# Optimization experiments

Hardware: AMD Instinct MI355X
Metric: run time of the kernel (lower is better)

## Reference

```python
import jax, jax.numpy as jnp
import numpy as np

B, L, G, D = 4096, 64, 8, 128
N_ITEMS, N_USERS, N_RATINGS = 100000, 50000, 5


def setup_inputs() -> dict:
    key = jax.random.key(0)
    ks = jax.random.split(key, 16)
    s = jnp.float32(0.02)
    return dict(
        nodes=jax.random.randint(ks[0], (B, G), 0, N_USERS),
        history_u=jax.random.randint(ks[1], (B, L), 0, N_ITEMS),
        history_r=jax.random.randint(ks[2], (B, L), 0, N_RATINGS),
        hist_len=jax.random.randint(ks[3], (B,), 0, L),
        v2e_weight=jax.random.normal(ks[4], (N_ITEMS, D), dtype=jnp.float32) * s,
        u2e_weight=jax.random.normal(ks[5], (N_USERS, D), dtype=jnp.float32) * s,
        r2e_weight=jax.random.normal(ks[6], (N_RATINGS, D), dtype=jnp.float32) * s,
        W1=jax.random.normal(ks[7], (2 * D, D), dtype=jnp.float32) * s,
        b1=jnp.zeros((D,), jnp.float32),
        W2=jax.random.normal(ks[8], (D, D), dtype=jnp.float32) * s,
        b2=jnp.zeros((D,), jnp.float32),
        att1_W=jax.random.normal(ks[9], (2 * D, D), dtype=jnp.float32) * s,
        att1_b=jnp.zeros((D,), jnp.float32),
        att2_W=jax.random.normal(ks[10], (D, D), dtype=jnp.float32) * s,
        att2_b=jnp.zeros((D,), jnp.float32),
        att3_W=jax.random.normal(ks[11], (D, 1), dtype=jnp.float32) * s,
        att3_b=jnp.zeros((1,), jnp.float32),
        ge_W=jax.random.normal(ks[12], (D, D), dtype=jnp.float32) * s,
        ge_b=jnp.zeros((D,), jnp.float32),
    )


def reference(nodes, history_u, history_r, hist_len,
              v2e_weight, u2e_weight, r2e_weight,
              W1, b1, W2, b2,
              att1_W, att1_b, att2_W, att2_b, att3_W, att3_b,
              ge_W, ge_b):
    lengths = hist_len + 1                      # ensure >=1 valid history entry per group
    e_uv = v2e_weight[history_u]                # [B, L, D] item-history gather
    e_r = r2e_weight[history_r]                 # [B, L, D] rating gather
    members = u2e_weight[nodes]                 # [B, G, D] member gather
    # Group_Embedding: pool members to one rep per group
    g = jax.nn.relu(members.mean(axis=1) @ ge_W + ge_b)            # [B, D]
    # per-history 2-layer MLP (w_r1, w_r2)
    x = jax.nn.relu(jnp.concatenate([e_uv, e_r], axis=-1) @ W1 + b1)
    o = jax.nn.relu(x @ W2 + b2)                # [B, L, D] o_history
    # Attention: cat(o_history, group_rep) -> relu -> relu -> scalar, softmax over L
    g_rep = jnp.broadcast_to(g[:, None, :], o.shape)               # [B, L, D]
    a = jax.nn.relu(jnp.concatenate([o, g_rep], axis=-1) @ att1_W + att1_b)
    a = jax.nn.relu(a @ att2_W + att2_b)
    logits = (a @ att3_W + att3_b)[..., 0]      # [B, L]
    mask = jnp.arange(L)[None, :] < lengths[:, None]
    logits = jnp.where(mask, logits, jnp.float32(-1e9))
    att = jax.nn.softmax(logits, axis=-1) * mask                   # ragged masked softmax
    # torch.mm(o_history.t(), att_w).t() == attention-weighted reduce over L
    return jnp.einsum('bl,bld->bd', att, o)     # [B, D]
```

## Files before the change

### kernel.cpp

```cpp
#include <hip/hip_runtime.h>
#include <hip/hip_bf16.h>

#define DD 128
#define TILE_BYTES 32768
#define WS_R_OFF   196608
#define WS_GB_OFF  199168

typedef __attribute__((ext_vector_type(8))) short bf16x8;
typedef __attribute__((ext_vector_type(4))) float f32x4;

__device__ inline unsigned short f2bf(float f) {
  unsigned u = __float_as_uint(f);
  return (unsigned short)((u + 0x7fffu + ((u >> 16) & 1u)) >> 16);
}

__device__ inline void async16(void* ldsp, const void* gp) {
  __builtin_amdgcn_global_load_lds(
      (const __attribute__((address_space(1))) void*)gp,
      (__attribute__((address_space(3))) void*)ldsp, 16, 0, 0);
}

__device__ inline void fill_w(char* slot, const char* src, int tid) {
  int w = tid >> 6, lane = tid & 63;
  #pragma unroll
  for (int i = 0; i < 8; ++i) {
    int ofs = ((i << 2) + w) << 10;
    async16(slot + ofs, src + ofs + lane * 16);
  }
}

__device__ inline bf16x8 ldfrag(const char* buf, int rowbase, int kk, int lane) {
  int row = rowbase + (lane & 15);
  int off = (row << 8) + (kk << 6) + (lane & 48);
  off ^= (row & 7) << 4;
  return *(const bf16x8*)(buf + off);
}

__device__ inline bf16x8 ldAg(const float* rp, int kk, int lane) {
  const float4* p = (const float4*)(rp + (kk << 5) + ((lane >> 4) << 3));
  float4 f0 = p[0], f1 = p[1];
  bf16x8 r;
  r[0] = (short)f2bf(f0.x); r[1] = (short)f2bf(f0.y);
  r[2] = (short)f2bf(f0.z); r[3] = (short)f2bf(f0.w);
  r[4] = (short)f2bf(f1.x); r[5] = (short)f2bf(f1.y);
  r[6] = (short)f2bf(f1.z); r[7] = (short)f2bf(f1.w);
  return r;
}

__device__ inline uint2 pack4(float v0, float v1, float v2, float v3) {
  return make_uint2((unsigned)f2bf(v0) | ((unsigned)f2bf(v1) << 16),
                    (unsigned)f2bf(v2) | ((unsigned)f2bf(v3) << 16));
}

#define MFMA(a, b, c) __builtin_amdgcn_mfma_f32_16x16x32_bf16((a), (b), (c), 0, 0, 0)

__global__ __launch_bounds__(256) void prep_weights(
    const float* __restrict__ W1, const float* __restrict__ W2,
    const float* __restrict__ a1W, const float* __restrict__ a2W,
    const float* __restrict__ geW,
    const float* __restrict__ r2e, const float* __restrict__ b1,
    unsigned short* __restrict__ wsw, float* __restrict__ Rp) {
  int gid = blockIdx.x * 256 + threadIdx.x;
  if (gid < 12288) {
    int tile = gid >> 11, idx = gid & 2047;
    int row = idx >> 4, slot = idx & 15;
    int slot2 = slot ^ (row & 7);
    const float* W; int kb;
    switch (tile) {
      case 0:  W = W1;  kb = 0;   break;
      case 1:  W = W2;  kb = 0;   break;
      case 2:  W = a1W; kb = 0;   break;
      case 3:  W = a2W; kb = 0;   break;
      case 4:  W = geW; kb = 0;   break;
      default: W = a1W; kb = 128; break;
    }
    unsigned pk[4];
    #pragma unroll
    for (int p = 0; p < 4; ++p) {
      unsigned short lo = f2bf(W[(size_t)(kb + slot2 * 8 + 2 * p) * DD + row]);
      unsigned short hi = f2bf(W[(size_t)(kb + slot2 * 8 + 2 * p + 1) * DD + row]);
      pk[p] = (unsigned)lo | ((unsigned)hi << 16);
    }
    *(uint4*)(wsw + (size_t)tile * 16384 + (size_t)idx * 8) =
        make_uint4(pk[0], pk[1], pk[2], pk[3]);
  } else {
    int t = gid - 12288;
    for (int idx = t; idx < 640; idx += 256) {
      int r = idx >> 7, d = idx & 127;
      float s = b1[d];
      for (int k = 0; k < 128; ++k)
        s = fmaf(r2e[r * DD + k], W1[(size_t)(DD + k) * DD + d], s);
      Rp[idx] = s;
    }
  }
}

__global__ __launch_bounds__(256, 2) void prep_gb(
    const int* __restrict__ nodes, const float* __restrict__ u2e,
    const float* __restrict__ geb, const float* __restrict__ a1b,
    const char* __restrict__ tiles, float* __restrict__ gbv) {
  __shared__ char mean_s[4096];
  __shared__ char g_s[4096];
  __shared__ char wslot[32768];
  __shared__ int nodes_s[128];
  int tid = threadIdx.x, w = tid >> 6, lane = tid & 63;
  int b0 = blockIdx.x * 16;
  if (tid < 128) nodes_s[tid] = nodes[b0 * 8 + tid];
  fill_w(wslot, tiles + 4 * TILE_BYTES, tid);
  __syncthreads();
  for (int idx = tid; idx < 2048; idx += 256) {
    int row = idx >> 7, d = idx & 127;
    float m = 0.f;
    #pragma unroll
    for (int j = 0; j < 8; ++j)
      m += u2e[(size_t)nodes_s[row * 8 + j] * DD + d];
    m *= 0.125f;
    int off = ((row << 8) + (d << 1)) ^ ((row & 7) << 4);
    *(unsigned short*)(mean_s + off) = f2bf(m);
  }
  __syncthreads();
  int cb = lane & 15, rb = (lane >> 4) << 2;
  f32x4 acc[2] = {(f32x4)(0.f), (f32x4)(0.f)};
  #pragma unroll
  for (int kk = 0; kk < 4; ++kk) {
    bf16x8 a = ldfrag(mean_s, 0, kk, lane);
    #pragma unroll
    for (int nf = 0; nf < 2; ++nf) {
      bf16x8 b = ldfrag(wslot, w * 32 + nf * 16, kk, lane);
      acc[nf] = MFMA(a, b, acc[nf]);
    }
  }
  __syncthreads();
  fill_w(wslot, tiles + 5 * TILE_BYTES, tid);
  #pragma unroll
  for (int nf = 0; nf < 2; ++nf) {
    int col = w * 32 + nf * 16 + cb;
    float gb2 = geb[col];
    #pragma unroll
    for (int j = 0; j < 4; ++j) {
      int row = rb + j;
      float v = fmaxf(acc[nf][j] + gb2, 0.f);
      int off = ((row << 8) + (col << 1)) ^ ((row & 7) << 4);
      *(unsigned short*)(g_s + off) = f2bf(v);
    }
  }
  __syncthreads();
  acc[0] = (f32x4)(0.f); acc[1] = (f32x4)(0.f);
  #pragma unroll
  for (int kk = 0; kk < 4; ++kk) {
    bf16x8 a = ldfrag(g_s, 0, kk, lane);
    #pragma unroll
    for (int nf = 0; nf < 2; ++nf) {
      bf16x8 b = ldfrag(wslot, w * 32 + nf * 16, kk, lane);
      acc[nf] = MFMA(a, b, acc[nf]);
    }
  }
  #pragma unroll
  for (int nf = 0; nf < 2; ++nf) {
    int col = w * 32 + nf * 16 + cb;
    float bb = a1b[col];
    #pragma unroll
    for (int j = 0; j < 4; ++j)
      gbv[(size_t)(b0 + rb + j) * DD + col] = acc[nf][j] + bb;
  }
}

__device__ inline void gemmWX(f32x4 acc[8], const char* Wt, const char* Xt,
                              int mfw, int nlw, int lane) {
  #pragma unroll
  for (int kk = 0; kk < 4; ++kk) {
    bf16x8 bf0 = ldfrag(Xt, nlw * 32, kk, lane);
    bf16x8 bf1 = ldfrag(Xt, nlw * 32 + 16, kk, lane);
    #pragma unroll
    for (int mf = 0; mf < 4; ++mf) {
      bf16x8 a = ldfrag(Wt, mfw * 64 + mf * 16, kk, lane);
      acc[mf * 2]     = MFMA(a, bf0, acc[mf * 2]);
      acc[mf * 2 + 1] = MFMA(a, bf1, acc[mf * 2 + 1]);
    }
  }
}

__global__ __launch_bounds__(512, 1) void main_kernel(
    const int* __restrict__ hu, const int* __restrict__ hr,
    const int* __restrict__ hlen,
    const float* __restrict__ v2e,
    const float* __restrict__ b2, const float* __restrict__ a2b,
    const float* __restrict__ a3W, const float* __restrict__ a3b,
    const char* __restrict__ tiles, const float* __restrict__ Rp,
    const float* __restrict__ gbv, float* __restrict__ out) {
  __shared__ char smem[163840];
  char* W1s = smem;
  char* W2s = smem + 32768;
  char* A1s = smem + 65536;
  char* A2s = smem + 98304;
  char* XA  = smem + 131072;
  char* XB  = smem + 147456;

  const int tid = threadIdx.x, lane = tid & 63;
  const int wv = tid >> 6;
  const int rowsel = wv >> 2;
  const int w4 = wv & 3;
  const int mfw = w4 >> 1, nlw = w4 & 1;
  const int cb = lane & 15, g = lane >> 4;
  char* X = rowsel ? XB : XA;

  #pragma unroll
  for (int i = 0; i < 4; ++i) {
    int ofs = (i * 8 + wv) << 10;
    async16(W1s + ofs, tiles + ofs + lane * 16);
    async16(W2s + ofs, tiles + TILE_BYTES + ofs + lane * 16);
    async16(A1s + ofs, tiles + 2 * TILE_BYTES + ofs + lane * 16);
    async16(A2s + ofs, tiles + 3 * TILE_BYTES + ofs + lane * 16);
  }
  const float a3bv = a3b[0];

  const int l0 = nlw * 32 + cb, l1 = l0 + 16;
  const int rbase = blockIdx.x * 16;
  int r = rbase + rowsel;
  int hu0 = hu[r * 64 + l0], hu1 = hu[r * 64 + l1];
  int hr0 = hr[r * 64 + l0], hr1 = hr[r * 64 + l1];
  __syncthreads();

  for (int p = 0; p < 8; ++p) {
    int hu0n = 0, hu1n = 0, hr0n = 0, hr1n = 0;
    if (p < 7) {
      int rn = r + 2;
      hu0n = hu[rn * 64 + l0]; hu1n = hu[rn * 64 + l1];
      hr0n = hr[rn * 64 + l0]; hr1n = hr[rn * 64 + l1];
    }

    f32x4 acc[8];
    #pragma unroll
    for (int i = 0; i < 8; ++i) acc[i] = (f32x4)(0.f);

    {
      const float* rp0 = v2e + (size_t)hu0 * DD;
      const float* rp1 = v2e + (size_t)hu1 * DD;
      #pragma unroll
      for (int kk = 0; kk < 4; ++kk) {
        bf16x8 bf0 = ldAg(rp0, kk, lane);
        bf16x8 bf1 = ldAg(rp1, kk, lane);
        #pragma unroll
        for (int mf = 0; mf < 4; ++mf) {
          bf16x8 a = ldfrag(W1s, mfw * 64 + mf * 16, kk, lane);
          acc[mf * 2]     = MFMA(a, bf0, acc[mf * 2]);
          acc[mf * 2 + 1] = MFMA(a, bf1, acc[mf * 2 + 1]);
        }
      }
    }
    #pragma unroll
    for (int mf = 0; mf < 4; ++mf) {
      int f0 = mfw * 64 + mf * 16 + g * 4;
      float4 r0 = *(const float4*)(Rp + hr0 * DD + f0);
      float4 r1 = *(const float4*)(Rp + hr1 * DD + f0);
      f32x4 v0 = acc[mf * 2], v1 = acc[mf * 2 + 1];
      uint2 p0 = pack4(fmaxf(v0[0] + r0.x, 0.f), fmaxf(v0[1] + r0.y, 0.f),
                       fmaxf(v0[2] + r0.z, 0.f), fmaxf(v0[3] + r0.w, 0.f));
      uint2 p1 = pack4(fmaxf(v1[0] + r1.x, 0.f), fmaxf(v1[1] + r1.y, 0.f),
                       fmaxf(v1[2] + r1.z, 0.f), fmaxf(v1[3] + r1.w, 0.f));
      int o0 = ((l0 << 8) + (f0 << 1)) ^ ((l0 & 7) << 4);
      int o1 = ((l1 << 8) + (f0 << 1)) ^ ((l1 & 7) << 4);
      *(uint2*)(X + o0) = p0;
      *(uint2*)(X + o1) = p1;
    }
    __syncthreads();

    #pragma unroll
    for (int i = 0; i < 8; ++i) acc[i] = (f32x4)(0.f);
    gemmWX(acc, W2s, X, mfw, nlw, lane);
    __syncthreads();
    uint2 opk[8];
    #pragma unroll
    for (int mf = 0; mf < 4; ++mf) {
      int f0 = mfw * 64 + mf * 16 + g * 4;
      float4 bb = *(const float4*)(b2 + f0);
      f32x4 v0 = acc[mf * 2], v1 = acc[mf * 2 + 1];
      uint2 p0 = pack4(fmaxf(v0[0] + bb.x, 0.f), fmaxf(v0[1] + bb.y, 0.f),
                       fmaxf(v0[2] + bb.z, 0.f), fmaxf(v0[3] + bb.w, 0.f));
      uint2 p1 = pack4(fmaxf(v1[0] + bb.x, 0.f), fmaxf(v1[1] + bb.y, 0.f),
                       fmaxf(v1[2] + bb.z, 0.f), fmaxf(v1[3] + bb.w, 0.f));
      opk[mf * 2] = p0; opk[mf * 2 + 1] = p1;
      int o0 = ((l0 << 8) + (f0 << 1)) ^ ((l0 & 7) << 4);
      int o1 = ((l1 << 8) + (f0 << 1)) ^ ((l1 & 7) << 4);
      *(uint2*)(X + o0) = p0;
      *(uint2*)(X + o1) = p1;
    }
    __syncthreads();

    #pragma unroll
    for (int i = 0; i < 8; ++i) acc[i] = (f32x4)(0.f);
    gemmWX(acc, A1s, X, mfw, nlw, lane);
    __syncthreads();
    #pragma unroll
    for (int mf = 0; mf < 4; ++mf) {
      int f0 = mfw * 64 + mf * 16 + g * 4;
      float4 gv = *(const float4*)(gbv + (size_t)r * DD + f0);
      f32x4 v0 = acc[mf * 2], v1 = acc[mf * 2 + 1];
      uint2 p0 = pack4(fmaxf(v0[0] + gv.x, 0.f), fmaxf(v0[1] + gv.y, 0.f),
                       fmaxf(v0[2] + gv.z, 0.f), fmaxf(v0[3] + gv.w, 0.f));
      uint2 p1 = pack4(fmaxf(v1[0] + gv.x, 0.f), fmaxf(v1[1] + gv.y, 0.f),
                       fmaxf(v1[2] + gv.z, 0.f), fmaxf(v1[3] + gv.w, 0.f));
      int o0 = ((l0 << 8) + (f0 << 1)) ^ ((l0 & 7) << 4);
      int o1 = ((l1 << 8) + (f0 << 1)) ^ ((l1 & 7) << 4);
      *(uint2*)(X + o0) = p0;
      *(uint2*)(X + o1) = p1;
    }
    __syncthreads();

    #pragma unroll
    for (int i = 0; i < 8; ++i) acc[i] = (f32x4)(0.f);
    gemmWX(acc, A2s, X, mfw, nlw, lane);
    __syncthreads();

    {
      float s0 = 0.f, s1 = 0.f;
      #pragma unroll
      for (int mf = 0; mf < 4; ++mf) {
        int f0 = mfw * 64 + mf * 16 + g * 4;
        float4 ab = *(const float4*)(a2b + f0);
        float4 aw = *(const float4*)(a3W + f0);
        f32x4 v0 = acc[mf * 2], v1 = acc[mf * 2 + 1];
        s0 = fmaf(fmaxf(v0[0] + ab.x, 0.f), aw.x, s0);
        s0 = fmaf(fmaxf(v0[1] + ab.y, 0.f), aw.y, s0);
        s0 = fmaf(fmaxf(v0[2] + ab.z, 0.f), aw.z, s0);
        s0 = fmaf(fmaxf(v0[3] + ab.w, 0.f), aw.w, s0);
        s1 = fmaf(fmaxf(v1[0] + ab.x, 0.f), aw.x, s1);
        s1 = fmaf(fmaxf(v1[1] + ab.y, 0.f), aw.y, s1);
        s1 = fmaf(fmaxf(v1[2] + ab.z, 0.f), aw.z, s1);
        s1 = fmaf(fmaxf(v1[3] + ab.w, 0.f), aw.w, s1);
      }
      s0 += __shfl_xor(s0, 16); s0 += __shfl_xor(s0, 32);
      s1 += __shfl_xor(s1, 16); s1 += __shfl_xor(s1, 32);
      if (g == 0) {
        *(float*)(X + mfw * 256 + l0 * 4) = s0;
        *(float*)(X + mfw * 256 + l1 * 4) = s1;
      }
    }
    __syncthreads();

    if (w4 == 0) {
      int l = lane;
      float lv = *(const float*)(X + l * 4) + *(const float*)(X + 256 + l * 4) + a3bv;
      int len = hlen[r] + 1;
      bool valid = l < len;
      if (!valid) lv = -1e30f;
      float m = lv;
      #pragma unroll
      for (int off = 32; off; off >>= 1) m = fmaxf(m, __shfl_xor(m, off));
      float pe = valid ? expf(lv - m) : 0.f;
      float s = pe;
      #pragma unroll
      for (int off = 32; off; off >>= 1) s += __shfl_xor(s, off);
      *(float*)(X + 512 + l * 4) = pe / s;
    }
    __syncthreads();

    {
      float att0 = *(const float*)(X + 512 + l0 * 4);
      float att1 = *(const float*)(X + 512 + l1 * 4);
      float pr[4][4];
      #pragma unroll
      for (int mf = 0; mf < 4; ++mf) {
        uint2 q0 = opk[mf * 2], q1 = opk[mf * 2 + 1];
        pr[mf][0] = att0 * __uint_as_float(q0.x << 16)
                  + att1 * __uint_as_float(q1.x << 16);
        pr[mf][1] = att0 * __uint_as_float(q0.x & 0xffff0000u)
                  + att1 * __uint_as_float(q1.x & 0xffff0000u);
        pr[mf][2] = att0 * __uint_as_float(q0.y << 16)
                  + att1 * __uint_as_float(q1.y << 16);
        pr[mf][3] = att0 * __uint_as_float(q0.y & 0xffff0000u)
                  + att1 * __uint_as_float(q1.y & 0xffff0000u);
      }
      #pragma unroll
      for (int m = 1; m < 16; m <<= 1) {
        #pragma unroll
        for (int mf = 0; mf < 4; ++mf) {
          pr[mf][0] += __shfl_xor(pr[mf][0], m);
          pr[mf][1] += __shfl_xor(pr[mf][1], m);
          pr[mf][2] += __shfl_xor(pr[mf][2], m);
          pr[mf][3] += __shfl_xor(pr[mf][3], m);
        }
      }
      if (cb == 0) {
        #pragma unroll
        for (int mf = 0; mf < 4; ++mf) {
          int f0 = mfw * 64 + mf * 16 + g * 4;
          float* rd = (float*)(X + 1024 + nlw * 512);
          rd[f0 + 0] = pr[mf][0];
          rd[f0 + 1] = pr[mf][1];
          rd[f0 + 2] = pr[mf][2];
          rd[f0 + 3] = pr[mf][3];
        }
      }
    }
    __syncthreads();

    if (tid < 128 || (tid >= 256 && tid < 384)) {
      int d = tid & 127;
      out[(size_t)r * DD + d] = *(const float*)(X + 1024 + d * 4)
                              + *(const float*)(X + 1536 + d * 4);
    }
    __syncthreads();

    hu0 = hu0n; hu1 = hu1n; hr0 = hr0n; hr1 = hr1n;
    r += 2;
  }
}

extern "C" void kernel_launch(void* const* d_in, const int* in_sizes, int n_in,
                              void* d_out, int out_size, void* d_ws, size_t ws_size,
                              hipStream_t stream) {
  const int*   nodes = (const int*)d_in[0];
  const int*   hu    = (const int*)d_in[1];
  const int*   hr    = (const int*)d_in[2];
  const int*   hlen  = (const int*)d_in[3];
  const float* v2e   = (const float*)d_in[4];
  const float* u2e   = (const float*)d_in[5];
  const float* r2e   = (const float*)d_in[6];
  const float* W1    = (const float*)d_in[7];
  const float* b1    = (const float*)d_in[8];
  const float* W2    = (const float*)d_in[9];
  const float* b2    = (const float*)d_in[10];
  const float* a1W   = (const float*)d_in[11];
  const float* a1b   = (const float*)d_in[12];
  const float* a2W   = (const float*)d_in[13];
  const float* a2b   = (const float*)d_in[14];
  const float* a3W   = (const float*)d_in[15];
  const float* a3b   = (const float*)d_in[16];
  const float* geW   = (const float*)d_in[17];
  const float* geb   = (const float*)d_in[18];
  float* out = (float*)d_out;

  unsigned short* wsw = (unsigned short*)d_ws;
  const char* tiles = (const char*)d_ws;
  float* Rp  = (float*)((char*)d_ws + WS_R_OFF);
  float* gbv = (float*)((char*)d_ws + WS_GB_OFF);

  prep_weights<<<49, 256, 0, stream>>>(W1, W2, a1W, a2W, geW, r2e, b1, wsw, Rp);
  prep_gb<<<256, 256, 0, stream>>>(nodes, u2e, geb, a1b, tiles, gbv);
  main_kernel<<<256, 512, 0, stream>>>(
      hu, hr, hlen, v2e, b2, a2b, a3W, a3b, tiles, Rp, gbv, out);
}
```

Measured before the change: 121.3 us.

## Double block to 16 waves, split features per wave, compute softmax per wave

The main kernel now launches 1024 threads per block, so each row is handled by 8 waves that each own 32 output features instead of 64. This halves per-wave MFMA work and accumulator registers, giving the CU more waves to hide gather and LDS latency. Every wave now reduces the four partial logit slots and computes the masked softmax itself, then broadcasts the weights with shuffles, which removes one LDS round trip and one block barrier per iteration. The cost is redundant softmax work in every wave and the extra overhead of synchronising a larger block.

```diff
diff --git a/kernel.cpp b/kernel.cpp
--- a/kernel.cpp
+++ b/kernel.cpp
@@ -13,6 +13,8 @@
   unsigned u = __float_as_uint(f);
   return (unsigned short)((u + 0x7fffu + ((u >> 16) & 1u)) >> 16);
 }
+__device__ inline float bf2f_lo(unsigned v) { return __uint_as_float(v << 16); }
+__device__ inline float bf2f_hi(unsigned v) { return __uint_as_float(v & 0xffff0000u); }
 
 __device__ inline void async16(void* ldsp, const void* gp) {
   __builtin_amdgcn_global_load_lds(
@@ -165,22 +167,22 @@
   }
 }
 
-__device__ inline void gemmWX(f32x4 acc[8], const char* Wt, const char* Xt,
+__device__ inline void gemm32(f32x4 acc[4], const char* Wt, const char* Xt,
                               int mfw, int nlw, int lane) {
   #pragma unroll
   for (int kk = 0; kk < 4; ++kk) {
-    bf16x8 bf0 = ldfrag(Xt, nlw * 32, kk, lane);
-    bf16x8 bf1 = ldfrag(Xt, nlw * 32 + 16, kk, lane);
-    #pragma unroll
-    for (int mf = 0; mf < 4; ++mf) {
-      bf16x8 a = ldfrag(Wt, mfw * 64 + mf * 16, kk, lane);
-      acc[mf * 2]     = MFMA(a, bf0, acc[mf * 2]);
-      acc[mf * 2 + 1] = MFMA(a, bf1, acc[mf * 2 + 1]);
-    }
-  }
-}
-
-__global__ __launch_bounds__(512, 1) void main_kernel(
+    bf16x8 b0 = ldfrag(Xt, nlw * 32, kk, lane);
+    bf16x8 b1 = ldfrag(Xt, nlw * 32 + 16, kk, lane);
+    #pragma unroll
+    for (int mf = 0; mf < 2; ++mf) {
+      bf16x8 a = ldfrag(Wt, mfw * 32 + mf * 16, kk, lane);
+      acc[mf * 2]     = MFMA(a, b0, acc[mf * 2]);
+      acc[mf * 2 + 1] = MFMA(a, b1, acc[mf * 2 + 1]);
+    }
+  }
+}
+
+__global__ __launch_bounds__(1024, 4) void main_kernel(
     const int* __restrict__ hu, const int* __restrict__ hr,
     const int* __restrict__ hlen,
     const float* __restrict__ v2e,
@@ -198,15 +200,16 @@
 
   const int tid = threadIdx.x, lane = tid & 63;
   const int wv = tid >> 6;
-  const int rowsel = wv >> 2;
-  const int w4 = wv & 3;
-  const int mfw = w4 >> 1, nlw = w4 & 1;
+  const int rowsel = wv >> 3;
+  const int w8 = wv & 7;
+  const int mfw = w8 >> 1, nlw = w8 & 1;
   const int cb = lane & 15, g = lane >> 4;
+  const int fbase = mfw * 32;
   char* X = rowsel ? XB : XA;
 
   #pragma unroll
-  for (int i = 0; i < 4; ++i) {
-    int ofs = (i * 8 + wv) << 10;
+  for (int i = 0; i < 2; ++i) {
+    int ofs = ((i << 4) + wv) << 10;
     async16(W1s + ofs, tiles + ofs + lane * 16);
     async16(W2s + ofs, tiles + TILE_BYTES + ofs + lane * 16);
     async16(A1s + ofs, tiles + 2 * TILE_BYTES + ofs + lane * 16);
@@ -215,8 +218,7 @@
   const float a3bv = a3b[0];
 
   const int l0 = nlw * 32 + cb, l1 = l0 + 16;
-  const int rbase = blockIdx.x * 16;
-  int r = rbase + rowsel;
+  int r = blockIdx.x * 16 + rowsel;
   int hu0 = hu[r * 64 + l0], hu1 = hu[r * 64 + l1];
   int hr0 = hr[r * 64 + l0], hr1 = hr[r * 64 + l1];
   __syncthreads();
@@ -229,28 +231,28 @@
       hr0n = hr[rn * 64 + l0]; hr1n = hr[rn * 64 + l1];
     }
 
-    f32x4 acc[8];
-    #pragma unroll
-    for (int i = 0; i < 8; ++i) acc[i] = (f32x4)(0.f);
+    f32x4 acc[4];
+    #pragma unroll
+    for (int i = 0; i < 4; ++i) acc[i] = (f32x4)(0.f);
 
     {
       const float* rp0 = v2e + (size_t)hu0 * DD;
       const float* rp1 = v2e + (size_t)hu1 * DD;
       #pragma unroll
       for (int kk = 0; kk < 4; ++kk) {
-        bf16x8 bf0 = ldAg(rp0, kk, lane);
-        bf16x8 bf1 = ldAg(rp1, kk, lane);
+        bf16x8 b0 = ldAg(rp0, kk, lane);
+        bf16x8 b1 = ldAg(rp1, kk, lane);
         #pragma unroll
-        for (int mf = 0; mf < 4; ++mf) {
-          bf16x8 a = ldfrag(W1s, mfw * 64 + mf * 16, kk, lane);
-          acc[mf * 2]     = MFMA(a, bf0, acc[mf * 2]);
-          acc[mf * 2 + 1] = MFMA(a, bf1, acc[mf * 2 + 1]);
+        for (int mf = 0; mf < 2; ++mf) {
+          bf16x8 a = ldfrag(W1s, fbase + mf * 16, kk, lane);
+          acc[mf * 2]     = MFMA(a, b0, acc[mf * 2]);
+          acc[mf * 2 + 1] = MFMA(a, b1, acc[mf * 2 + 1]);
         }
       }
     }
     #pragma unroll
-    for (int mf = 0; mf < 4; ++mf) {
-      int f0 = mfw * 64 + mf * 16 + g * 4;
+    for (int mf = 0; mf < 2; ++mf) {
+      int f0 = fbase + mf * 16 + g * 4;
       float4 r0 = *(const float4*)(Rp + hr0 * DD + f0);
       float4 r1 = *(const float4*)(Rp + hr1 * DD + f0);
       f32x4 v0 = acc[mf * 2], v1 = acc[mf * 2 + 1];
@@ -266,13 +268,13 @@
     __syncthreads();
 
     #pragma unroll
-    for (int i = 0; i < 8; ++i) acc[i] = (f32x4)(0.f);
-    gemmWX(acc, W2s, X, mfw, nlw, lane);
-    __syncthreads();
-    uint2 opk[8];
-    #pragma unroll
-    for (int mf = 0; mf < 4; ++mf) {
-      int f0 = mfw * 64 + mf * 16 + g * 4;
+    for (int i = 0; i < 4; ++i) acc[i] = (f32x4)(0.f);
+    gemm32(acc, W2s, X, mfw, nlw, lane);
+    __syncthreads();
+    uint2 opk[4];
+    #pragma unroll
+    for (int mf = 0; mf < 2; ++mf) {
+      int f0 = fbase + mf * 16 + g * 4;
       float4 bb = *(const float4*)(b2 + f0);
       f32x4 v0 = acc[mf * 2], v1 = acc[mf * 2 + 1];
       uint2 p0 = pack4(fmaxf(v0[0] + bb.x, 0.f), fmaxf(v0[1] + bb.y, 0.f),
@@ -288,12 +290,12 @@
     __syncthreads();
 
     #pragma unroll
-    for (int i = 0; i < 8; ++i) acc[i] = (f32x4)(0.f);
-    gemmWX(acc, A1s, X, mfw, nlw, lane);
-    __syncthreads();
-    #pragma unroll
-    for (int mf = 0; mf < 4; ++mf) {
-      int f0 = mfw * 64 + mf * 16 + g * 4;
+    for (int i = 0; i < 4; ++i) acc[i] = (f32x4)(0.f);
+    gemm32(acc, A1s, X, mfw, nlw, lane);
+    __syncthreads();
+    #pragma unroll
+    for (int mf = 0; mf < 2; ++mf) {
+      int f0 = fbase + mf * 16 + g * 4;
       float4 gv = *(const float4*)(gbv + (size_t)r * DD + f0);
       f32x4 v0 = acc[mf * 2], v1 = acc[mf * 2 + 1];
       uint2 p0 = pack4(fmaxf(v0[0] + gv.x, 0.f), fmaxf(v0[1] + gv.y, 0.f),
@@ -308,15 +310,15 @@
     __syncthreads();
 
     #pragma unroll
-    for (int i = 0; i < 8; ++i) acc[i] = (f32x4)(0.f);
-    gemmWX(acc, A2s, X, mfw, nlw, lane);
+    for (int i = 0; i < 4; ++i) acc[i] = (f32x4)(0.f);
+    gemm32(acc, A2s, X, mfw, nlw, lane);
     __syncthreads();
 
     {
       float s0 = 0.f, s1 = 0.f;
       #pragma unroll
-      for (int mf = 0; mf < 4; ++mf) {
-        int f0 = mfw * 64 + mf * 16 + g * 4;
+      for (int mf = 0; mf < 2; ++mf) {
+        int f0 = fbase + mf * 16 + g * 4;
         float4 ab = *(const float4*)(a2b + f0);
         float4 aw = *(const float4*)(a3W + f0);
         f32x4 v0 = acc[mf * 2], v1 = acc[mf * 2 + 1];
@@ -338,9 +340,12 @@
     }
     __syncthreads();
 
-    if (w4 == 0) {
+    float att0, att1;
+    {
       int l = lane;
-      float lv = *(const float*)(X + l * 4) + *(const float*)(X + 256 + l * 4) + a3bv;
+      float lv = *(const float*)(X + l * 4) + *(const float*)(X + 256 + l * 4)
+               + *(const float*)(X + 512 + l * 4) + *(const float*)(X + 768 + l * 4)
+               + a3bv;
       int len = hlen[r] + 1;
       bool valid = l < len;
       if (!valid) lv = -1e30f;
@@ -351,30 +356,25 @@
       float s = pe;
       #pragma unroll
       for (int off = 32; off; off >>= 1) s += __shfl_xor(s, off);
-      *(float*)(X + 512 + l * 4) = pe / s;
-    }
-    __syncthreads();
+      float att = pe / s;
+      att0 = __shfl(att, l0);
+      att1 = __shfl(att, l1);
+    }
 
     {
-      float att0 = *(const float*)(X + 512 + l0 * 4);
-      float att1 = *(const float*)(X + 512 + l1 * 4);
-      float pr[4][4];
-      #pragma unroll
-      for (int mf = 0; mf < 4; ++mf) {
+      float pr[2][4];
+      #pragma unroll
+      for (int mf = 0; mf < 2; ++mf) {
         uint2 q0 = opk[mf * 2], q1 = opk[mf * 2 + 1];
-        pr[mf][0] = att0 * __uint_as_float(q0.x << 16)
-                  + att1 * __uint_as_float(q1.x << 16);
-        pr[mf][1] = att0 * __uint_as_float(q0.x & 0xffff0000u)
-                  + att1 * __uint_as_float(q1.x & 0xffff0000u);
-        pr[mf][2] = att0 * __uint_as_float(q0.y << 16)
-                  + att1 * __uint_as_float(q1.y << 16);
-        pr[mf][3] = att0 * __uint_as_float(q0.y & 0xffff0000u)
-                  + att1 * __uint_as_float(q1.y & 0xffff0000u);
+        pr[mf][0] = att0 * bf2f_lo(q0.x) + att1 * bf2f_lo(q1.x);
+        pr[mf][1] = att0 * bf2f_hi(q0.x) + att1 * bf2f_hi(q1.x);
+        pr[mf][2] = att0 * bf2f_lo(q0.y) + att1 * bf2f_lo(q1.y);
+        pr[mf][3] = att0 * bf2f_hi(q0.y) + att1 * bf2f_hi(q1.y);
       }
       #pragma unroll
       for (int m = 1; m < 16; m <<= 1) {
         #pragma unroll
-        for (int mf = 0; mf < 4; ++mf) {
+        for (int mf = 0; mf < 2; ++mf) {
           pr[mf][0] += __shfl_xor(pr[mf][0], m);
           pr[mf][1] += __shfl_xor(pr[mf][1], m);
           pr[mf][2] += __shfl_xor(pr[mf][2], m);
@@ -382,10 +382,10 @@
         }
       }
       if (cb == 0) {
+        float* rd = (float*)(X + 1024 + nlw * 512);
         #pragma unroll
-        for (int mf = 0; mf < 4; ++mf) {
-          int f0 = mfw * 64 + mf * 16 + g * 4;
-          float* rd = (float*)(X + 1024 + nlw * 512);
+        for (int mf = 0; mf < 2; ++mf) {
+          int f0 = fbase + mf * 16 + g * 4;
           rd[f0 + 0] = pr[mf][0];
           rd[f0 + 1] = pr[mf][1];
           rd[f0 + 2] = pr[mf][2];
@@ -395,7 +395,7 @@
     }
     __syncthreads();
 
-    if (tid < 128 || (tid >= 256 && tid < 384)) {
+    if ((tid & 511) < 128) {
       int d = tid & 127;
       out[(size_t)r * DD + d] = *(const float*)(X + 1024 + d * 4)
                               + *(const float*)(X + 1536 + d * 4);
@@ -438,6 +438,6 @@
 
   prep_weights<<<49, 256, 0, stream>>>(W1, W2, a1W, a2W, geW, r2e, b1, wsw, Rp);
   prep_gb<<<256, 256, 0, stream>>>(nodes, u2e, geb, a1b, tiles, gbv);
-  main_kernel<<<256, 512, 0, stream>>>(
+  main_kernel<<<256, 1024, 0, stream>>>(
       hu, hr, hlen, v2e, b2, a2b, a3W, a3b, tiles, Rp, gbv, out);
 }
```

Measured after the change: 159.4 us. 1.31x slower.

## Process four rows per pass with double-buffered weight slots and wider wave tiles

Applied to the files above, without the earlier changes.

Each wave pair now owns a whole row of 64 history entries, and each wave computes a 64x64 output tile with 16 accumulators instead of 8. Four rows are processed per iteration instead of two. The four 32KB weight tiles no longer stay resident in LDS. Two slots are refilled asynchronously between GEMM stages, which cuts LDS use and avoids splitting the L dimension across waves. The trade is more register pressure, weight reloads on every iteration, and a cross-wave dot-product reduction replaced by simpler per-row reductions.

```diff
diff --git a/kernel.cpp b/kernel.cpp
--- a/kernel.cpp
+++ b/kernel.cpp
@@ -13,6 +13,8 @@
   unsigned u = __float_as_uint(f);
   return (unsigned short)((u + 0x7fffu + ((u >> 16) & 1u)) >> 16);
 }
+__device__ inline float bf2f_lo(unsigned v) { return __uint_as_float(v << 16); }
+__device__ inline float bf2f_hi(unsigned v) { return __uint_as_float(v & 0xffff0000u); }
 
 __device__ inline void async16(void* ldsp, const void* gp) {
   __builtin_amdgcn_global_load_lds(
@@ -25,6 +27,15 @@
   #pragma unroll
   for (int i = 0; i < 8; ++i) {
     int ofs = ((i << 2) + w) << 10;
+    async16(slot + ofs, src + ofs + lane * 16);
+  }
+}
+
+__device__ inline void fill512(char* slot, const char* src, int tid) {
+  int w = tid >> 6, lane = tid & 63;
+  #pragma unroll
+  for (int i = 0; i < 4; ++i) {
+    int ofs = ((i << 3) + w) << 10;
     async16(slot + ofs, src + ofs + lane * 16);
   }
 }
@@ -165,17 +176,19 @@
   }
 }
 
-__device__ inline void gemmWX(f32x4 acc[8], const char* Wt, const char* Xt,
-                              int mfw, int nlw, int lane) {
+__device__ inline void gemm64(f32x4 acc[16], const char* Wt, const char* Xt,
+                              int wf, int lane) {
   #pragma unroll
   for (int kk = 0; kk < 4; ++kk) {
-    bf16x8 bf0 = ldfrag(Xt, nlw * 32, kk, lane);
-    bf16x8 bf1 = ldfrag(Xt, nlw * 32 + 16, kk, lane);
+    bf16x8 b[4];
+    #pragma unroll
+    for (int nf = 0; nf < 4; ++nf) b[nf] = ldfrag(Xt, nf * 16, kk, lane);
     #pragma unroll
     for (int mf = 0; mf < 4; ++mf) {
-      bf16x8 a = ldfrag(Wt, mfw * 64 + mf * 16, kk, lane);
-      acc[mf * 2]     = MFMA(a, bf0, acc[mf * 2]);
-      acc[mf * 2 + 1] = MFMA(a, bf1, acc[mf * 2 + 1]);
+      bf16x8 a = ldfrag(Wt, wf * 64 + mf * 16, kk, lane);
+      #pragma unroll
+      for (int nf = 0; nf < 4; ++nf)
+        acc[mf * 4 + nf] = MFMA(a, b[nf], acc[mf * 4 + nf]);
     }
   }
 }
@@ -188,159 +201,150 @@
     const float* __restrict__ a3W, const float* __restrict__ a3b,
     const char* __restrict__ tiles, const float* __restrict__ Rp,
     const float* __restrict__ gbv, float* __restrict__ out) {
-  __shared__ char smem[163840];
-  char* W1s = smem;
-  char* W2s = smem + 32768;
-  char* A1s = smem + 65536;
-  char* A2s = smem + 98304;
-  char* XA  = smem + 131072;
-  char* XB  = smem + 147456;
+  __shared__ char smem[136192];
+  char* slotA = smem;
+  char* slotB = smem + 32768;
+  char* Xall  = smem + 65536;
+  float* lpart = (float*)(smem + 131072);
+  float* att_s = (float*)(smem + 131072 + 2048);
+  float* red   = (float*)(smem + 131072 + 3072);
 
   const int tid = threadIdx.x, lane = tid & 63;
   const int wv = tid >> 6;
-  const int rowsel = wv >> 2;
-  const int w4 = wv & 3;
-  const int mfw = w4 >> 1, nlw = w4 & 1;
+  const int ri = wv >> 1;
+  const int wf = wv & 1;
   const int cb = lane & 15, g = lane >> 4;
-  char* X = rowsel ? XB : XA;
-
-  #pragma unroll
-  for (int i = 0; i < 4; ++i) {
-    int ofs = (i * 8 + wv) << 10;
-    async16(W1s + ofs, tiles + ofs + lane * 16);
-    async16(W2s + ofs, tiles + TILE_BYTES + ofs + lane * 16);
-    async16(A1s + ofs, tiles + 2 * TILE_BYTES + ofs + lane * 16);
-    async16(A2s + ofs, tiles + 3 * TILE_BYTES + ofs + lane * 16);
-  }
+  char* X = Xall + ri * 16384;
   const float a3bv = a3b[0];
 
-  const int l0 = nlw * 32 + cb, l1 = l0 + 16;
-  const int rbase = blockIdx.x * 16;
-  int r = rbase + rowsel;
-  int hu0 = hu[r * 64 + l0], hu1 = hu[r * 64 + l1];
-  int hr0 = hr[r * 64 + l0], hr1 = hr[r * 64 + l1];
+  fill512(slotA, tiles, tid);
+  fill512(slotB, tiles + TILE_BYTES, tid);
   __syncthreads();
 
-  for (int p = 0; p < 8; ++p) {
-    int hu0n = 0, hu1n = 0, hr0n = 0, hr1n = 0;
-    if (p < 7) {
-      int rn = r + 2;
-      hu0n = hu[rn * 64 + l0]; hu1n = hu[rn * 64 + l1];
-      hr0n = hr[rn * 64 + l0]; hr1n = hr[rn * 64 + l1];
-    }
-
-    f32x4 acc[8];
-    #pragma unroll
-    for (int i = 0; i < 8; ++i) acc[i] = (f32x4)(0.f);
-
+  for (int it = 0; it < 4; ++it) {
+    const int r = blockIdx.x * 16 + it * 4 + ri;
+    int hu_l[4], hr_l[4];
+    #pragma unroll
+    for (int nf = 0; nf < 4; ++nf) {
+      hu_l[nf] = hu[r * 64 + nf * 16 + cb];
+      hr_l[nf] = hr[r * 64 + nf * 16 + cb];
+    }
+
+    f32x4 acc[16];
+    #pragma unroll
+    for (int i = 0; i < 16; ++i) acc[i] = (f32x4)(0.f);
+
+    #pragma unroll
+    for (int kk = 0; kk < 4; ++kk) {
+      bf16x8 b[4];
+      #pragma unroll
+      for (int nf = 0; nf < 4; ++nf)
+        b[nf] = ldAg(v2e + (size_t)hu_l[nf] * DD, kk, lane);
+      #pragma unroll
+      for (int mf = 0; mf < 4; ++mf) {
+        bf16x8 a = ldfrag(slotA, wf * 64 + mf * 16, kk, lane);
+        #pragma unroll
+        for (int nf = 0; nf < 4; ++nf)
+          acc[mf * 4 + nf] = MFMA(a, b[nf], acc[mf * 4 + nf]);
+      }
+    }
+    #pragma unroll
+    for (int mf = 0; mf < 4; ++mf) {
+      int f0 = wf * 64 + mf * 16 + g * 4;
+      #pragma unroll
+      for (int nf = 0; nf < 4; ++nf) {
+        float4 rr = *(const float4*)(Rp + hr_l[nf] * DD + f0);
+        f32x4 v = acc[mf * 4 + nf];
+        uint2 pv = pack4(fmaxf(v[0] + rr.x, 0.f), fmaxf(v[1] + rr.y, 0.f),
+                         fmaxf(v[2] + rr.z, 0.f), fmaxf(v[3] + rr.w, 0.f));
+        int l0 = nf * 16 + cb;
+        int off = ((l0 << 8) + (f0 << 1)) ^ ((l0 & 7) << 4);
+        *(uint2*)(X + off) = pv;
+      }
+    }
+    __syncthreads();
+    fill512(slotA, tiles + 2 * TILE_BYTES, tid);
+
+    #pragma unroll
+    for (int i = 0; i < 16; ++i) acc[i] = (f32x4)(0.f);
+    gemm64(acc, slotB, X, wf, lane);
+    __syncthreads();
+    fill512(slotB, tiles + 3 * TILE_BYTES, tid);
+    uint2 opk[16];
+    #pragma unroll
+    for (int mf = 0; mf < 4; ++mf) {
+      int f0 = wf * 64 + mf * 16 + g * 4;
+      float4 bb = *(const float4*)(b2 + f0);
+      #pragma unroll
+      for (int nf = 0; nf < 4; ++nf) {
+        f32x4 v = acc[mf * 4 + nf];
+        uint2 pv = pack4(fmaxf(v[0] + bb.x, 0.f), fmaxf(v[1] + bb.y, 0.f),
+                         fmaxf(v[2] + bb.z, 0.f), fmaxf(v[3] + bb.w, 0.f));
+        opk[mf * 4 + nf] = pv;
+        int l0 = nf * 16 + cb;
+        int off = ((l0 << 8) + (f0 << 1)) ^ ((l0 & 7) << 4);
+        *(uint2*)(X + off) = pv;
+      }
+    }
+    __syncthreads();
+
+    #pragma unroll
+    for (int i = 0; i < 16; ++i) acc[i] = (f32x4)(0.f);
+    gemm64(acc, slotA, X, wf, lane);
+    __syncthreads();
+    fill512(slotA, tiles, tid);
+    #pragma unroll
+    for (int mf = 0; mf < 4; ++mf) {
+      int f0 = wf * 64 + mf * 16 + g * 4;
+      float4 gv = *(const float4*)(gbv + (size_t)r * DD + f0);
+      #pragma unroll
+      for (int nf = 0; nf < 4; ++nf) {
+        f32x4 v = acc[mf * 4 + nf];
+        uint2 pv = pack4(fmaxf(v[0] + gv.x, 0.f), fmaxf(v[1] + gv.y, 0.f),
+                         fmaxf(v[2] + gv.z, 0.f), fmaxf(v[3] + gv.w, 0.f));
+        int l0 = nf * 16 + cb;
+        int off = ((l0 << 8) + (f0 << 1)) ^ ((l0 & 7) << 4);
+        *(uint2*)(X + off) = pv;
+      }
+    }
+    __syncthreads();
+
+    #pragma unroll
+    for (int i = 0; i < 16; ++i) acc[i] = (f32x4)(0.f);
+    gemm64(acc, slotB, X, wf, lane);
     {
-      const float* rp0 = v2e + (size_t)hu0 * DD;
-      const float* rp1 = v2e + (size_t)hu1 * DD;
-      #pragma unroll
-      for (int kk = 0; kk < 4; ++kk) {
-        bf16x8 bf0 = ldAg(rp0, kk, lane);
-        bf16x8 bf1 = ldAg(rp1, kk, lane);
-        #pragma unroll
-        for (int mf = 0; mf < 4; ++mf) {
-          bf16x8 a = ldfrag(W1s, mfw * 64 + mf * 16, kk, lane);
-          acc[mf * 2]     = MFMA(a, bf0, acc[mf * 2]);
-          acc[mf * 2 + 1] = MFMA(a, bf1, acc[mf * 2 + 1]);
-        }
-      }
-    }
-    #pragma unroll
-    for (int mf = 0; mf < 4; ++mf) {
-      int f0 = mfw * 64 + mf * 16 + g * 4;
-      float4 r0 = *(const float4*)(Rp + hr0 * DD + f0);
-      float4 r1 = *(const float4*)(Rp + hr1 * DD + f0);
-      f32x4 v0 = acc[mf * 2], v1 = acc[mf * 2 + 1];
-      uint2 p0 = pack4(fmaxf(v0[0] + r0.x, 0.f), fmaxf(v0[1] + r0.y, 0.f),
-                       fmaxf(v0[2] + r0.z, 0.f), fmaxf(v0[3] + r0.w, 0.f));
-      uint2 p1 = pack4(fmaxf(v1[0] + r1.x, 0.f), fmaxf(v1[1] + r1.y, 0.f),
-                       fmaxf(v1[2] + r1.z, 0.f), fmaxf(v1[3] + r1.w, 0.f));
-      int o0 = ((l0 << 8) + (f0 << 1)) ^ ((l0 & 7) << 4);
-      int o1 = ((l1 << 8) + (f0 << 1)) ^ ((l1 & 7) << 4);
-      *(uint2*)(X + o0) = p0;
-      *(uint2*)(X + o1) = p1;
-    }
-    __syncthreads();
-
-    #pragma unroll
-    for (int i = 0; i < 8; ++i) acc[i] = (f32x4)(0.f);
-    gemmWX(acc, W2s, X, mfw, nlw, lane);
-    __syncthreads();
-    uint2 opk[8];
-    #pragma unroll
-    for (int mf = 0; mf < 4; ++mf) {
-      int f0 = mfw * 64 + mf * 16 + g * 4;
-      float4 bb = *(const float4*)(b2 + f0);
-      f32x4 v0 = acc[mf * 2], v1 = acc[mf * 2 + 1];
-      uint2 p0 = pack4(fmaxf(v0[0] + bb.x, 0.f), fmaxf(v0[1] + bb.y, 0.f),
-                       fmaxf(v0[2] + bb.z, 0.f), fmaxf(v0[3] + bb.w, 0.f));
-      uint2 p1 = pack4(fmaxf(v1[0] + bb.x, 0.f), fmaxf(v1[1] + bb.y, 0.f),
-                       fmaxf(v1[2] + bb.z, 0.f), fmaxf(v1[3] + bb.w, 0.f));
-      opk[mf * 2] = p0; opk[mf * 2 + 1] = p1;
-      int o0 = ((l0 << 8) + (f0 << 1)) ^ ((l0 & 7) << 4);
-      int o1 = ((l1 << 8) + (f0 << 1)) ^ ((l1 & 7) << 4);
-      *(uint2*)(X + o0) = p0;
-      *(uint2*)(X + o1) = p1;
-    }
-    __syncthreads();
-
-    #pragma unroll
-    for (int i = 0; i < 8; ++i) acc[i] = (f32x4)(0.f);
-    gemmWX(acc, A1s, X, mfw, nlw, lane);
-    __syncthreads();
-    #pragma unroll
-    for (int mf = 0; mf < 4; ++mf) {
-      int f0 = mfw * 64 + mf * 16 + g * 4;
-      float4 gv = *(const float4*)(gbv + (size_t)r * DD + f0);
-      f32x4 v0 = acc[mf * 2], v1 = acc[mf * 2 + 1];
-      uint2 p0 = pack4(fmaxf(v0[0] + gv.x, 0.f), fmaxf(v0[1] + gv.y, 0.f),
-                       fmaxf(v0[2] + gv.z, 0.f), fmaxf(v0[3] + gv.w, 0.f));
-      uint2 p1 = pack4(fmaxf(v1[0] + gv.x, 0.f), fmaxf(v1[1] + gv.y, 0.f),
-                       fmaxf(v1[2] + gv.z, 0.f), fmaxf(v1[3] + gv.w, 0.f));
-      int o0 = ((l0 << 8) + (f0 << 1)) ^ ((l0 & 7) << 4);
-      int o1 = ((l1 << 8) + (f0 << 1)) ^ ((l1 & 7) << 4);
-      *(uint2*)(X + o0) = p0;
-      *(uint2*)(X + o1) = p1;
-    }
-    __syncthreads();
-
-    #pragma unroll
-    for (int i = 0; i < 8; ++i) acc[i] = (f32x4)(0.f);
-    gemmWX(acc, A2s, X, mfw, nlw, lane);
-    __syncthreads();
-
-    {
-      float s0 = 0.f, s1 = 0.f;
+      float s[4] = {0.f, 0.f, 0.f, 0.f};
       #pragma unroll
       for (int mf = 0; mf < 4; ++mf) {
-        int f0 = mfw * 64 + mf * 16 + g * 4;
+        int f0 = wf * 64 + mf * 16 + g * 4;
         float4 ab = *(const float4*)(a2b + f0);
         float4 aw = *(const float4*)(a3W + f0);
-        f32x4 v0 = acc[mf * 2], v1 = acc[mf * 2 + 1];
-        s0 = fmaf(fmaxf(v0[0] + ab.x, 0.f), aw.x, s0);
-        s0 = fmaf(fmaxf(v0[1] + ab.y, 0.f), aw.y, s0);
-        s0 = fmaf(fmaxf(v0[2] + ab.z, 0.f), aw.z, s0);
-        s0 = fmaf(fmaxf(v0[3] + ab.w, 0.f), aw.w, s0);
-        s1 = fmaf(fmaxf(v1[0] + ab.x, 0.f), aw.x, s1);
-        s1 = fmaf(fmaxf(v1[1] + ab.y, 0.f), aw.y, s1);
-        s1 = fmaf(fmaxf(v1[2] + ab.z, 0.f), aw.z, s1);
-        s1 = fmaf(fmaxf(v1[3] + ab.w, 0.f), aw.w, s1);
-      }
-      s0 += __shfl_xor(s0, 16); s0 += __shfl_xor(s0, 32);
-      s1 += __shfl_xor(s1, 16); s1 += __shfl_xor(s1, 32);
+        #pragma unroll
+        for (int nf = 0; nf < 4; ++nf) {
+          f32x4 v = acc[mf * 4 + nf];
+          s[nf] = fmaf(fmaxf(v[0] + ab.x, 0.f), aw.x, s[nf]);
+          s[nf] = fmaf(fmaxf(v[1] + ab.y, 0.f), aw.y, s[nf]);
+          s[nf] = fmaf(fmaxf(v[2] + ab.z, 0.f), aw.z, s[nf]);
+          s[nf] = fmaf(fmaxf(v[3] + ab.w, 0.f), aw.w, s[nf]);
+        }
+      }
+      #pragma unroll
+      for (int nf = 0; nf < 4; ++nf) {
+        s[nf] += __shfl_xor(s[nf], 16);
+        s[nf] += __shfl_xor(s[nf], 32);
+      }
       if (g == 0) {
-        *(float*)(X + mfw * 256 + l0 * 4) = s0;
-        *(float*)(X + mfw * 256 + l1 * 4) = s1;
-      }
-    }
-    __syncthreads();
-
-    if (w4 == 0) {
+        #pragma unroll
+        for (int nf = 0; nf < 4; ++nf)
+          lpart[ri * 128 + wf * 64 + nf * 16 + cb] = s[nf];
+      }
+    }
+    __syncthreads();
+    fill512(slotB, tiles + TILE_BYTES, tid);
+
+    if (wf == 0) {
       int l = lane;
-      float lv = *(const float*)(X + l * 4) + *(const float*)(X + 256 + l * 4) + a3bv;
+      float lv = lpart[ri * 128 + l] + lpart[ri * 128 + 64 + l] + a3bv;
       int len = hlen[r] + 1;
       bool valid = l < len;
       if (!valid) lv = -1e30f;
@@ -348,28 +352,29 @@
       #pragma unroll
       for (int off = 32; off; off >>= 1) m = fmaxf(m, __shfl_xor(m, off));
       float pe = valid ? expf(lv - m) : 0.f;
-      float s = pe;
-      #pragma unroll
-      for (int off = 32; off; off >>= 1) s += __shfl_xor(s, off);
-      *(float*)(X + 512 + l * 4) = pe / s;
+      float su = pe;
+      #pragma unroll
+      for (int off = 32; off; off >>= 1) su += __shfl_xor(su, off);
+      att_s[ri * 64 + l] = pe / su;
     }
     __syncthreads();
 
     {
-      float att0 = *(const float*)(X + 512 + l0 * 4);
-      float att1 = *(const float*)(X + 512 + l1 * 4);
+      float att[4];
+      #pragma unroll
+      for (int nf = 0; nf < 4; ++nf) att[nf] = att_s[ri * 64 + nf * 16 + cb];
       float pr[4][4];
       #pragma unroll
       for (int mf = 0; mf < 4; ++mf) {
-        uint2 q0 = opk[mf * 2], q1 = opk[mf * 2 + 1];
-        pr[mf][0] = att0 * __uint_as_float(q0.x << 16)
-                  + att1 * __uint_as_float(q1.x << 16);
-        pr[mf][1] = att0 * __uint_as_float(q0.x & 0xffff0000u)
-                  + att1 * __uint_as_float(q1.x & 0xffff0000u);
-        pr[mf][2] = att0 * __uint_as_float(q0.y << 16)
-                  + att1 * __uint_as_float(q1.y << 16);
-        pr[mf][3] = att0 * __uint_as_float(q0.y & 0xffff0000u)
-                  + att1 * __uint_as_float(q1.y & 0xffff0000u);
+        pr[mf][0] = 0.f; pr[mf][1] = 0.f; pr[mf][2] = 0.f; pr[mf][3] = 0.f;
+        #pragma unroll
+        for (int nf = 0; nf < 4; ++nf) {
+          uint2 q = opk[mf * 4 + nf];
+          pr[mf][0] = fmaf(att[nf], bf2f_lo(q.x), pr[mf][0]);
+          pr[mf][1] = fmaf(att[nf], bf2f_hi(q.x), pr[mf][1]);
+          pr[mf][2] = fmaf(att[nf], bf2f_lo(q.y), pr[mf][2]);
+          pr[mf][3] = fmaf(att[nf], bf2f_hi(q.y), pr[mf][3]);
+        }
       }
       #pragma unroll
       for (int m = 1; m < 16; m <<= 1) {
@@ -384,26 +389,19 @@
       if (cb == 0) {
         #pragma unroll
         for (int mf = 0; mf < 4; ++mf) {
-          int f0 = mfw * 64 + mf * 16 + g * 4;
-          float* rd = (float*)(X + 1024 + nlw * 512);
-          rd[f0 + 0] = pr[mf][0];
-          rd[f0 + 1] = pr[mf][1];
-          rd[f0 + 2] = pr[mf][2];
-          rd[f0 + 3] = pr[mf][3];
+          int f0 = wf * 64 + mf * 16 + g * 4;
+          *(float4*)(red + ri * 128 + f0) =
+              make_float4(pr[mf][0], pr[mf][1], pr[mf][2], pr[mf][3]);
         }
       }
     }
     __syncthreads();
 
-    if (tid < 128 || (tid >= 256 && tid < 384)) {
-      int d = tid & 127;
-      out[(size_t)r * DD + d] = *(const float*)(X + 1024 + d * 4)
-                              + *(const float*)(X + 1536 + d * 4);
-    }
-    __syncthreads();
-
-    hu0 = hu0n; hu1 = hu1n; hr0 = hr0n; hr1 = hr1n;
-    r += 2;
+    {
+      int r2 = tid >> 7, d = tid & 127;
+      out[(size_t)(blockIdx.x * 16 + it * 4 + r2) * DD + d] = red[r2 * 128 + d];
+    }
+    __syncthreads();
   }
 }
 
```

After: 173.9 us. 1.43x slower.
